# Optimization experiments

Hardware: AMD Instinct MI355X
Metric: run time of the kernel (lower is better)

## Reference

```python
import jax, jax.numpy as jnp
import numpy as np

BATCH, K, N, D = 8192, 8, 1024, 256
BETA = 0.25


def setup_inputs() -> dict:
    key = jax.random.key(0)
    kx, ke = jax.random.split(key)
    x = jax.random.normal(kx, (BATCH, K, D), dtype=jnp.float32)
    entries = jax.random.normal(ke, (K, N, D), dtype=jnp.float32)
    return {"x": x, "entries": entries}


def reference(x, entries):
    # x: [b, k, d]; entries: [k, n, d]
    xt = jnp.transpose(x, (1, 0, 2))  # [k, b, d]
    # squared euclidean distances (argmin is identical to cdist argmin)
    d2 = (
        jnp.sum(xt * xt, axis=-1)[:, :, None]
        + jnp.sum(entries * entries, axis=-1)[:, None, :]
        - 2.0 * jnp.einsum("kbd,knd->kbn", xt, entries)
    )  # [k, b, n]
    idx = jnp.argmin(d2, axis=-1)  # [k, b]
    quantized = jnp.take_along_axis(entries, idx[:, :, None], axis=1)  # [k, b, d]
    quantized = jnp.transpose(quantized, (1, 0, 2))  # [b, k, d]
    # straight-through estimator
    x_q = x + jax.lax.stop_gradient(quantized - x)
    dictionary_loss = jnp.mean(
        jnp.sum((jax.lax.stop_gradient(x) - quantized) ** 2, axis=-1)
    )
    commitment_loss = BETA * jnp.mean(
        jnp.sum((x - jax.lax.stop_gradient(quantized)) ** 2, axis=-1)
    )
    return x_q, jnp.transpose(idx, (1, 0)), dictionary_loss, commitment_loss
```

## Files before the change

kernel.cpp:

```cpp
#include <hip/hip_runtime.h>
#include <cstdint>
#include <cstddef>

#define BATCH 8192
#define KC 8
#define NC 1024
#define DC 256
#define TAU 0.10f

typedef __attribute__((ext_vector_type(8))) _Float16 half8;
typedef __attribute__((ext_vector_type(4))) _Float16 half4;
typedef __attribute__((ext_vector_type(4))) float floatx4;

__device__ __forceinline__ void async_load16(const void* g, void* l) {
    __builtin_amdgcn_global_load_lds((const __attribute__((address_space(1))) uint32_t*)g,
                                     (__attribute__((address_space(3))) uint32_t*)l, 16, 0, 0);
}

__device__ __forceinline__ int lidx(int r, int c) {
    return (r >> 3) * 1024 + (r & 7) * 128 + ((c ^ (r & 7)) * 16);
}
__device__ __forceinline__ half8 ldsr(const char* base, int r, int c) {
    return *(const half8*)(base + lidx(r, c));
}

__global__ __launch_bounds__(256) void prep_e_kernel(const float* __restrict__ entries,
                                                     _Float16* __restrict__ Ecat,
                                                     float* __restrict__ eef) {
    int wave = threadIdx.x >> 6, lane = threadIdx.x & 63;
    int row = blockIdx.x * 4 + wave;
    float4 v = ((const float4*)(entries + (size_t)row * DC))[lane];
    half4 h;
    h.x = (_Float16)v.x; h.y = (_Float16)v.y; h.z = (_Float16)v.z; h.w = (_Float16)v.w;
    *(half4*)(Ecat + (size_t)row * 256 + lane * 4) = h;
    double s = (double)v.x * v.x + (double)v.y * v.y + (double)v.z * v.z + (double)v.w * v.w;
    #pragma unroll
    for (int off = 32; off > 0; off >>= 1) s += __shfl_down(s, off, 64);
    if (lane == 0) eef[row] = (float)s;
}

__global__ __launch_bounds__(256, 2) void vq_gemm(const float* __restrict__ x,
                                                  const float* __restrict__ entries,
                                                  const _Float16* __restrict__ Ecat,
                                                  const float* __restrict__ eef,
                                                  float* __restrict__ out_idx,
                                                  float* __restrict__ out_q,
                                                  double* __restrict__ partial,
                                                  int* __restrict__ flag_list,
                                                  int* __restrict__ flag_cnt) {
    __shared__ alignas(16) char Bst[2][32768];
    __shared__ float eef_lds[NC];
    __shared__ float tv1[128];
    __shared__ float tv2[128];
    __shared__ int   ti1[128];
    __shared__ int   idx_lds[128];
    __shared__ double red[256];

    const int t = threadIdx.x;
    const int k  = blockIdx.x & 7;
    const int b0 = (blockIdx.x >> 3) * 128;
    const int w = t >> 6, lane = t & 63;
    const int quad = lane >> 4, col = lane & 15;
    const int rl = lane >> 3;
    const int cs = (lane & 7) ^ rl;

    { float4 v = ((const float4*)(eef + (size_t)k * NC))[t]; *(float4*)(eef_lds + t * 4) = v; }

    half8 Ah[2][8];
    #pragma unroll
    for (int mi = 0; mi < 2; ++mi) {
        const float* xrow = x + ((size_t)(b0 + w * 32 + mi * 16 + col) * KC + k) * DC + quad * 8;
        #pragma unroll
        for (int ks = 0; ks < 8; ++ks) {
            float4 u0 = *(const float4*)(xrow + ks * 32);
            float4 u1 = *(const float4*)(xrow + ks * 32 + 4);
            float f[8] = {u0.x, u0.y, u0.z, u0.w, u1.x, u1.y, u1.z, u1.w};
            half8 h;
            #pragma unroll
            for (int j = 0; j < 8; ++j) h[j] = (_Float16)f[j];
            Ah[mi][ks] = h;
        }
    }

    const char* EcatK = (const char*)(Ecat + (size_t)k * NC * 256);

    #define ISSUE_B(nt_, h_)                                                             \
        {                                                                                \
            char* bb_ = Bst[h_];                                                         \
            _Pragma("unroll")                                                            \
            for (int j = 0; j < 8; ++j) {                                                \
                int li_ = w * 8 + j; int sub_ = li_ >> 4, grp_ = li_ & 15;               \
                const char* src_ = EcatK + (size_t)((nt_) * 128 + grp_ * 8 + rl) * 512   \
                                 + ((h_) * 128 + sub_ * 64) * 2 + cs * 16;               \
                async_load16(src_, bb_ + sub_ * 16384 + grp_ * 1024 + lane * 16);        \
            }                                                                            \
        }

    #define STAGE(h_, DOISS_, nti_)                                                      \
        {                                                                                \
            asm volatile("s_waitcnt vmcnt(0)" ::: "memory");                             \
            __builtin_amdgcn_s_barrier();                                                \
            __builtin_amdgcn_sched_barrier(0);                                           \
            if (DOISS_) { ISSUE_B((nti_), (h_) ^ 1); }                                   \
            const char* Bs_ = Bst[h_];                                                   \
            __builtin_amdgcn_s_setprio(1);                                               \
            _Pragma("unroll")                                                            \
            for (int sub = 0; sub < 2; ++sub) {                                          \
                _Pragma("unroll")                                                        \
                for (int kk = 0; kk < 2; ++kk) {                                         \
                    const int cb = kk * 4 + quad;                                        \
                    _Pragma("unroll")                                                    \
                    for (int ni = 0; ni < 8; ++ni) {                                     \
                        half8 bh = ldsr(Bs_ + sub * 16384, ni * 16 + col, cb);           \
                        acc[0][ni] = __builtin_amdgcn_mfma_f32_16x16x32_f16(             \
                            Ah[0][(h_) * 4 + sub * 2 + kk], bh, acc[0][ni], 0, 0, 0);    \
                        acc[1][ni] = __builtin_amdgcn_mfma_f32_16x16x32_f16(             \
                            Ah[1][(h_) * 4 + sub * 2 + kk], bh, acc[1][ni], 0, 0, 0);    \
                    }                                                                    \
                }                                                                        \
            }                                                                            \
            __builtin_amdgcn_s_setprio(0);                                               \
        }

    float lv1[8], lv2[8]; int li1[8];
    #pragma unroll
    for (int q = 0; q < 8; ++q) { lv1[q] = 1e30f; lv2[q] = 1e30f; li1[q] = 0; }

    ISSUE_B(0, 0);

    for (int nt = 0; nt < 8; ++nt) {
        const int n0 = nt * 128;
        floatx4 acc[2][8] = {};
        STAGE(0, 1, nt)
        STAGE(1, (nt < 7), nt + 1)
        float ev[8];
        #pragma unroll
        for (int ni = 0; ni < 8; ++ni) ev[ni] = eef_lds[n0 + ni * 16 + col];
        #pragma unroll
        for (int mi = 0; mi < 2; ++mi) {
            #pragma unroll
            for (int reg = 0; reg < 4; ++reg) {
                const int q = mi * 4 + reg;
                #pragma unroll
                for (int ni = 0; ni < 8; ++ni) {
                    float val = fmaf(-2.0f, acc[mi][ni][reg], ev[ni]);
                    int n = n0 + ni * 16 + col;
                    bool lt1 = val < lv1[q];
                    bool lt2 = val < lv2[q];
                    float nv2 = lt1 ? lv1[q] : (lt2 ? val : lv2[q]);
                    li1[q] = lt1 ? n : li1[q];
                    lv1[q] = lt1 ? val : lv1[q];
                    lv2[q] = nv2;
                }
            }
        }
    }

    #pragma unroll
    for (int mi = 0; mi < 2; ++mi) {
        #pragma unroll
        for (int reg = 0; reg < 4; ++reg) {
            const int q = mi * 4 + reg;
            float v1 = lv1[q], v2 = lv2[q]; int i1 = li1[q];
            #pragma unroll
            for (int off = 1; off < 16; off <<= 1) {
                float o1 = __shfl_xor(v1, off, 16);
                float o2 = __shfl_xor(v2, off, 16);
                int   oi = __shfl_xor(i1, off, 16);
                bool sw = o1 < v1;
                float hi = sw ? v1 : o1;
                v1 = sw ? o1 : v1;
                i1 = sw ? oi : i1;
                v2 = fminf(fminf(v2, o2), hi);
            }
            if (col == 0) {
                int row = w * 32 + mi * 16 + quad * 4 + reg;
                tv1[row] = v1; tv2[row] = v2; ti1[row] = i1;
            }
        }
    }

    __syncthreads();
    if (t < 128) {
        float v1 = tv1[t], v2 = tv2[t];
        int rid = (b0 + t) * KC + k;
        if (v2 - v1 < TAU) {
            int pos = atomicAdd(&flag_cnt[k], 1);
            flag_list[k * 8192 + pos] = rid;
            idx_lds[t] = -1;
        } else {
            int n = ti1[t];
            idx_lds[t] = n;
            out_idx[rid] = (float)n;
        }
    }
    __syncthreads();

    double s = 0.0;
    #pragma unroll
    for (int rr = 0; rr < 8; ++rr) {
        int r = rr * 16 + (t >> 4);
        int c = t & 15;
        int n = idx_lds[r];
        if (n >= 0) {
            const float4* xp = (const float4*)(x + ((size_t)(b0 + r) * KC + k) * DC);
            const float4* ep = (const float4*)(entries + ((size_t)k * NC + n) * DC);
            float4* op = (float4*)(out_q + ((size_t)(b0 + r) * KC + k) * DC);
            #pragma unroll
            for (int j = 0; j < 4; ++j) {
                int ci = j * 16 + c;
                float4 xv = xp[ci], evv = ep[ci];
                op[ci] = evv;
                double d0 = (double)xv.x - evv.x, d1 = (double)xv.y - evv.y;
                double d2 = (double)xv.z - evv.z, d3 = (double)xv.w - evv.w;
                s += d0 * d0 + d1 * d1 + d2 * d2 + d3 * d3;
            }
        }
    }
    red[t] = s;
    __syncthreads();
    for (int off2 = 128; off2 > 0; off2 >>= 1) {
        if (t < off2) red[t] += red[t + off2];
        __syncthreads();
    }
    if (t == 0) partial[blockIdx.x] = red[0];
    #undef STAGE
    #undef ISSUE_B
}

__global__ __launch_bounds__(256) void refine_scan(const float* __restrict__ x,
                                                   const float* __restrict__ entries,
                                                   const int* __restrict__ flag_list,
                                                   const int* __restrict__ flag_cnt,
                                                   unsigned long long* __restrict__ slots) {
    __shared__ alignas(16) char tileb[128 * 256];
    __shared__ float xs[16 * 260];
    const int t = threadIdx.x;
    const int r = t >> 4, eg = t & 15;
    for (int it = blockIdx.x; it < 8 * 8 * 512; it += gridDim.x) {
        const int k = it & 7, seg = (it >> 3) & 7, g = it >> 6;
        const int cnt_k = flag_cnt[k];
        if (g * 16 >= cnt_k) continue;
        const int nrows = min(16, cnt_k - g * 16);
        const int myrow = (r < nrows) ? r : 0;
        const int rid = flag_list[k * 8192 + g * 16 + myrow];
        {
            const int rr = t >> 4, c16 = t & 15;
            const int rid2 = flag_list[k * 8192 + g * 16 + ((rr < nrows) ? rr : 0)];
            const float4* xp = (const float4*)(x + (size_t)rid2 * DC);
            #pragma unroll
            for (int j = 0; j < 4; ++j) {
                float4 v = xp[c16 * 4 + j];
                *(float4*)(xs + rr * 260 + (c16 * 4 + j) * 4) = v;
            }
        }
        double acc[8] = {};
        #pragma unroll
        for (int c = 0; c < 4; ++c) {
            {
                const int c16 = t & 15;
                #pragma unroll
                for (int it2 = 0; it2 < 8; ++it2) {
                    int row = it2 * 16 + (t >> 4);
                    float4 v = *(const float4*)(entries
                        + ((size_t)k * NC + seg * 128 + row) * DC + c * 64 + c16 * 4);
                    *(float4*)(tileb + row * 256 + ((c16 ^ (row >> 3)) * 16)) = v;
                }
            }
            __syncthreads();
            const float* xpp = xs + r * 260 + c * 64;
            #pragma unroll 4
            for (int dq = 0; dq < 16; ++dq) {
                float4 xv = *(const float4*)(xpp + dq * 4);
                #pragma unroll
                for (int j = 0; j < 8; ++j) {
                    int e = eg * 8 + j;
                    float4 evv = *(const float4*)(tileb + e * 256 + ((dq ^ eg) * 16));
                    double d0 = (double)xv.x - (double)evv.x;
                    double d1 = (double)xv.y - (double)evv.y;
                    double d2 = (double)xv.z - (double)evv.z;
                    double d3 = (double)xv.w - (double)evv.w;
                    acc[j] += d0 * d0 + d1 * d1 + d2 * d2 + d3 * d3;
                }
            }
            __syncthreads();
        }
        double best = acc[0]; int bn = seg * 128 + eg * 8;
        #pragma unroll
        for (int j = 1; j < 8; ++j) {
            if (acc[j] < best) { best = acc[j]; bn = seg * 128 + eg * 8 + j; }
        }
        unsigned long long key =
            ((unsigned long long)__double_as_longlong(best) & ~1023ull)
            | (unsigned long long)(unsigned)bn;
        #pragma unroll
        for (int off = 1; off < 16; off <<= 1) {
            unsigned long long o = __shfl_xor(key, off, 16);
            key = o < key ? o : key;
        }
        if (eg == 0 && r < nrows) {
            atomicMin(&slots[k * 8192 + g * 16 + r], key);
        }
        (void)rid;
    }
}

__global__ __launch_bounds__(256) void refine_pick(const float* __restrict__ entries,
                                                   const int* __restrict__ flag_list,
                                                   const int* __restrict__ flag_cnt,
                                                   const unsigned long long* __restrict__ slots,
                                                   float* __restrict__ out_idx,
                                                   float* __restrict__ out_q,
                                                   double* __restrict__ refAcc) {
    const int t = threadIdx.x;
    for (int idx = blockIdx.x; idx < 8 * 8192; idx += gridDim.x) {
        const int k = idx >> 13, pos = idx & 8191;
        if (pos >= flag_cnt[k]) continue;
        unsigned long long key = slots[idx];
        int n = (int)(key & 1023ull);
        int rid = flag_list[idx];
        out_q[(size_t)rid * DC + t] = entries[((size_t)k * NC + n) * DC + t];
        if (t == 0) {
            out_idx[rid] = (float)n;
            atomicAdd(refAcc, __longlong_as_double((long long)(key & ~1023ull)));
        }
    }
}

__global__ __launch_bounds__(256) void finalize_kernel(const double* __restrict__ partial,
                                                       const double* __restrict__ refAcc,
                                                       float* __restrict__ out) {
    __shared__ double red[256];
    const int t = threadIdx.x;
    double s = 0.0;
    for (int i = t; i < 512; i += 256) s += partial[i];
    red[t] = s;
    __syncthreads();
    for (int off = 128; off > 0; off >>= 1) {
        if (t < off) red[t] += red[t + off];
        __syncthreads();
    }
    if (t == 0) {
        double L = (red[0] + *refAcc) * (1.0 / 65536.0);
        out[(size_t)BATCH * KC * DC + BATCH * KC + 0] = (float)L;
        out[(size_t)BATCH * KC * DC + BATCH * KC + 1] = (float)(0.25 * L);
    }
}

extern "C" void kernel_launch(void* const* d_in, const int* in_sizes, int n_in,
                              void* d_out, int out_size, void* d_ws, size_t ws_size,
                              hipStream_t stream) {
    const float* x       = (const float*)d_in[0];
    const float* entries = (const float*)d_in[1];
    float* out = (float*)d_out;

    char* ws = (char*)d_ws;
    int*      flag_cnt  = (int*)ws;
    double*   refAcc    = (double*)(ws + 64);
    double*   partial   = (double*)(ws + 4096);
    float*    eef       = (float*)(ws + 65536);
    int*      flag_list = (int*)(ws + 131072);
    _Float16* Ecat      = (_Float16*)(ws + 1048576);
    unsigned long long* slots = (unsigned long long*)(ws + 5242880);

    float* out_q   = out;
    float* out_idx = out + (size_t)BATCH * KC * DC;

    hipMemsetAsync(ws, 0, 128, stream);
    hipMemsetAsync(slots, 0xFF, (size_t)65536 * 8, stream);
    prep_e_kernel<<<KC * NC / 4, 256, 0, stream>>>(entries, Ecat, eef);
    vq_gemm<<<512, 256, 0, stream>>>(x, entries, Ecat, eef, out_idx, out_q,
                                     partial, flag_list, flag_cnt);
    refine_scan<<<512, 256, 0, stream>>>(x, entries, flag_list, flag_cnt, slots);
    refine_pick<<<512, 256, 0, stream>>>(entries, flag_list, flag_cnt, slots,
                                         out_idx, out_q, refAcc);
    finalize_kernel<<<1, 256, 0, stream>>>(partial, refAcc, out);
}
```

Measured before the change: 225.9 us.

## Split codebook N across two blocks and resolve top-2 in a separate kernel

The GEMM kernel now covers half of the codebook per block, so the grid doubles to 1024 blocks. Shared memory per block is halved, allowing three blocks per CU instead of two. Each half writes its best candidate as a sortable key and atomically updates a global second-best minimum. A new resolve kernel merges the two halves, applies the ambiguity threshold, and writes the quantized output and loss partials. The aim is better occupancy and load balance, at the cost of an extra launch, an extra memset, and each block reloading the same x rows.

```diff
diff --git a/kernel.cpp b/kernel.cpp
--- a/kernel.cpp
+++ b/kernel.cpp
@@ -15,6 +15,14 @@
 __device__ __forceinline__ void async_load16(const void* g, void* l) {
     __builtin_amdgcn_global_load_lds((const __attribute__((address_space(1))) uint32_t*)g,
                                      (__attribute__((address_space(3))) uint32_t*)l, 16, 0, 0);
+}
+__device__ __forceinline__ unsigned sortable(float v) {
+    unsigned u = __float_as_uint(v);
+    return u ^ (unsigned)(((int)u >> 31) | 0x80000000);
+}
+__device__ __forceinline__ float unsortable(unsigned ks) {
+    unsigned u = (ks & 0x80000000u) ? (ks ^ 0x80000000u) : ~ks;
+    return __uint_as_float(u);
 }
 
 __device__ __forceinline__ int lidx(int r, int c) {
@@ -39,32 +47,26 @@
     if (lane == 0) eef[row] = (float)s;
 }
 
-__global__ __launch_bounds__(256, 2) void vq_gemm(const float* __restrict__ x,
-                                                  const float* __restrict__ entries,
+__global__ __launch_bounds__(256, 3) void vq_gemm(const float* __restrict__ x,
                                                   const _Float16* __restrict__ Ecat,
                                                   const float* __restrict__ eef,
-                                                  float* __restrict__ out_idx,
-                                                  float* __restrict__ out_q,
-                                                  double* __restrict__ partial,
-                                                  int* __restrict__ flag_list,
-                                                  int* __restrict__ flag_cnt) {
-    __shared__ alignas(16) char Bst[2][32768];
-    __shared__ float eef_lds[NC];
-    __shared__ float tv1[128];
-    __shared__ float tv2[128];
-    __shared__ int   ti1[128];
-    __shared__ int   idx_lds[128];
-    __shared__ double red[256];
+                                                  unsigned long long* __restrict__ s01,
+                                                  unsigned* __restrict__ g2min) {
+    __shared__ alignas(16) char Bst[2][16384];
+    __shared__ float eef_lds[512];
 
     const int t = threadIdx.x;
     const int k  = blockIdx.x & 7;
-    const int b0 = (blockIdx.x >> 3) * 128;
+    const int g  = blockIdx.x >> 3;
+    const int b0 = (g >> 1) * 128;
+    const int nh = g & 1;
+    const int ncol0 = nh * 512;
     const int w = t >> 6, lane = t & 63;
     const int quad = lane >> 4, col = lane & 15;
     const int rl = lane >> 3;
     const int cs = (lane & 7) ^ rl;
 
-    { float4 v = ((const float4*)(eef + (size_t)k * NC))[t]; *(float4*)(eef_lds + t * 4) = v; }
+    ((float2*)eef_lds)[t] = ((const float2*)(eef + (size_t)k * NC + ncol0))[t];
 
     half8 Ah[2][8];
     #pragma unroll
@@ -84,39 +86,37 @@
 
     const char* EcatK = (const char*)(Ecat + (size_t)k * NC * 256);
 
-    #define ISSUE_B(nt_, h_)                                                             \
+    #define ISSUE_B(nt_, ds_, buf_)                                                      \
         {                                                                                \
-            char* bb_ = Bst[h_];                                                         \
+            char* bb_ = Bst[buf_];                                                       \
             _Pragma("unroll")                                                            \
-            for (int j = 0; j < 8; ++j) {                                                \
-                int li_ = w * 8 + j; int sub_ = li_ >> 4, grp_ = li_ & 15;               \
-                const char* src_ = EcatK + (size_t)((nt_) * 128 + grp_ * 8 + rl) * 512   \
-                                 + ((h_) * 128 + sub_ * 64) * 2 + cs * 16;               \
-                async_load16(src_, bb_ + sub_ * 16384 + grp_ * 1024 + lane * 16);        \
+            for (int j = 0; j < 4; ++j) {                                                \
+                int grp_ = w * 4 + j;                                                    \
+                const char* src_ = EcatK                                                 \
+                    + (size_t)(ncol0 + (nt_) * 128 + grp_ * 8 + rl) * 512                \
+                    + (ds_) * 128 + cs * 16;                                             \
+                async_load16(src_, bb_ + grp_ * 1024 + lane * 16);                       \
             }                                                                            \
         }
 
-    #define STAGE(h_, DOISS_, nti_)                                                      \
+    #define STAGE(nt_, ds_, DOISS_, nnt_, nds_)                                          \
         {                                                                                \
             asm volatile("s_waitcnt vmcnt(0)" ::: "memory");                             \
             __builtin_amdgcn_s_barrier();                                                \
             __builtin_amdgcn_sched_barrier(0);                                           \
-            if (DOISS_) { ISSUE_B((nti_), (h_) ^ 1); }                                   \
-            const char* Bs_ = Bst[h_];                                                   \
+            if (DOISS_) { ISSUE_B((nnt_), (nds_), ((ds_) + 1) & 1); }                    \
+            const char* Bs_ = Bst[(ds_) & 1];                                            \
             __builtin_amdgcn_s_setprio(1);                                               \
             _Pragma("unroll")                                                            \
-            for (int sub = 0; sub < 2; ++sub) {                                          \
+            for (int kk = 0; kk < 2; ++kk) {                                             \
+                const int cb = kk * 4 + quad;                                            \
                 _Pragma("unroll")                                                        \
-                for (int kk = 0; kk < 2; ++kk) {                                         \
-                    const int cb = kk * 4 + quad;                                        \
-                    _Pragma("unroll")                                                    \
-                    for (int ni = 0; ni < 8; ++ni) {                                     \
-                        half8 bh = ldsr(Bs_ + sub * 16384, ni * 16 + col, cb);           \
-                        acc[0][ni] = __builtin_amdgcn_mfma_f32_16x16x32_f16(             \
-                            Ah[0][(h_) * 4 + sub * 2 + kk], bh, acc[0][ni], 0, 0, 0);    \
-                        acc[1][ni] = __builtin_amdgcn_mfma_f32_16x16x32_f16(             \
-                            Ah[1][(h_) * 4 + sub * 2 + kk], bh, acc[1][ni], 0, 0, 0);    \
-                    }                                                                    \
+                for (int ni = 0; ni < 8; ++ni) {                                         \
+                    half8 bh = ldsr(Bs_, ni * 16 + col, cb);                             \
+                    acc[0][ni] = __builtin_amdgcn_mfma_f32_16x16x32_f16(                 \
+                        Ah[0][(ds_) * 2 + kk], bh, acc[0][ni], 0, 0, 0);                 \
+                    acc[1][ni] = __builtin_amdgcn_mfma_f32_16x16x32_f16(                 \
+                        Ah[1][(ds_) * 2 + kk], bh, acc[1][ni], 0, 0, 0);                 \
                 }                                                                        \
             }                                                                            \
             __builtin_amdgcn_s_setprio(0);                                               \
@@ -126,13 +126,15 @@
     #pragma unroll
     for (int q = 0; q < 8; ++q) { lv1[q] = 1e30f; lv2[q] = 1e30f; li1[q] = 0; }
 
-    ISSUE_B(0, 0);
-
-    for (int nt = 0; nt < 8; ++nt) {
+    ISSUE_B(0, 0, 0);
+
+    for (int nt = 0; nt < 4; ++nt) {
         const int n0 = nt * 128;
         floatx4 acc[2][8] = {};
-        STAGE(0, 1, nt)
-        STAGE(1, (nt < 7), nt + 1)
+        STAGE(nt, 0, 1, nt, 1)
+        STAGE(nt, 1, 1, nt, 2)
+        STAGE(nt, 2, 1, nt, 3)
+        STAGE(nt, 3, (nt < 3), nt + 1, 0)
         float ev[8];
         #pragma unroll
         for (int ni = 0; ni < 8; ++ni) ev[ni] = eef_lds[n0 + ni * 16 + col];
@@ -157,39 +159,63 @@
     }
 
     #pragma unroll
-    for (int mi = 0; mi < 2; ++mi) {
-        #pragma unroll
-        for (int reg = 0; reg < 4; ++reg) {
-            const int q = mi * 4 + reg;
-            float v1 = lv1[q], v2 = lv2[q]; int i1 = li1[q];
-            #pragma unroll
-            for (int off = 1; off < 16; off <<= 1) {
-                float o1 = __shfl_xor(v1, off, 16);
-                float o2 = __shfl_xor(v2, off, 16);
-                int   oi = __shfl_xor(i1, off, 16);
-                bool sw = o1 < v1;
-                float hi = sw ? v1 : o1;
-                v1 = sw ? o1 : v1;
-                i1 = sw ? oi : i1;
-                v2 = fminf(fminf(v2, o2), hi);
-            }
-            if (col == 0) {
-                int row = w * 32 + mi * 16 + quad * 4 + reg;
-                tv1[row] = v1; tv2[row] = v2; ti1[row] = i1;
-            }
-        }
-    }
-
-    __syncthreads();
+    for (int q = 0; q < 8; ++q) {
+        float v1 = lv1[q], v2 = lv2[q]; int i1 = li1[q];
+        #pragma unroll
+        for (int off = 1; off < 16; off <<= 1) {
+            float o1 = __shfl_xor(v1, off, 16);
+            float o2 = __shfl_xor(v2, off, 16);
+            int   oi = __shfl_xor(i1, off, 16);
+            bool sw = o1 < v1;
+            float hi = sw ? v1 : o1;
+            v1 = sw ? o1 : v1;
+            i1 = sw ? oi : i1;
+            v2 = fminf(fminf(v2, o2), hi);
+        }
+        if (col == 0) {
+            const int mi = q >> 2, reg = q & 3;
+            int row = w * 32 + mi * 16 + quad * 4 + reg;
+            int rid = (b0 + row) * KC + k;
+            s01[(size_t)nh * 65536 + rid] =
+                ((unsigned long long)sortable(v1) << 32) | (unsigned)(ncol0 + i1);
+            atomicMin(&g2min[rid], sortable(v2));
+        }
+    }
+    #undef STAGE
+    #undef ISSUE_B
+}
+
+__global__ __launch_bounds__(256) void resolve_kernel(const float* __restrict__ x,
+                                                      const float* __restrict__ entries,
+                                                      const unsigned long long* __restrict__ s01,
+                                                      const unsigned* __restrict__ g2min,
+                                                      float* __restrict__ out_idx,
+                                                      float* __restrict__ out_q,
+                                                      double* __restrict__ partial,
+                                                      int* __restrict__ flag_list,
+                                                      int* __restrict__ flag_cnt) {
+    __shared__ int idx_lds[128];
+    __shared__ double red[256];
+    const int t = threadIdx.x;
+    const int r0 = blockIdx.x * 128;
+
     if (t < 128) {
-        float v1 = tv1[t], v2 = tv2[t];
-        int rid = (b0 + t) * KC + k;
+        int rid = r0 + t;
+        unsigned long long sa = s01[rid], sb = s01[65536 + rid];
+        unsigned long long lo = sa < sb ? sa : sb;
+        unsigned long long hi = sa < sb ? sb : sa;
+        unsigned v2u = g2min[rid];
+        unsigned hv = (unsigned)(hi >> 32);
+        if (hv < v2u) v2u = hv;
+        float v1 = unsortable((unsigned)(lo >> 32));
+        float v2 = unsortable(v2u);
         if (v2 - v1 < TAU) {
+            int k = rid & 7;
             int pos = atomicAdd(&flag_cnt[k], 1);
             flag_list[k * 8192 + pos] = rid;
             idx_lds[t] = -1;
         } else {
-            int n = ti1[t];
+            int n = (int)(lo & 0xFFFFFFFFull);
             idx_lds[t] = n;
             out_idx[rid] = (float)n;
         }
@@ -203,9 +229,10 @@
         int c = t & 15;
         int n = idx_lds[r];
         if (n >= 0) {
-            const float4* xp = (const float4*)(x + ((size_t)(b0 + r) * KC + k) * DC);
-            const float4* ep = (const float4*)(entries + ((size_t)k * NC + n) * DC);
-            float4* op = (float4*)(out_q + ((size_t)(b0 + r) * KC + k) * DC);
+            int rid2 = r0 + r;
+            const float4* xp = (const float4*)(x + (size_t)rid2 * DC);
+            const float4* ep = (const float4*)(entries + (((size_t)(rid2 & 7)) * NC + n) * DC);
+            float4* op = (float4*)(out_q + (size_t)rid2 * DC);
             #pragma unroll
             for (int j = 0; j < 4; ++j) {
                 int ci = j * 16 + c;
@@ -224,8 +251,6 @@
         __syncthreads();
     }
     if (t == 0) partial[blockIdx.x] = red[0];
-    #undef STAGE
-    #undef ISSUE_B
 }
 
 __global__ __launch_bounds__(256) void refine_scan(const float* __restrict__ x,
@@ -242,8 +267,6 @@
         const int cnt_k = flag_cnt[k];
         if (g * 16 >= cnt_k) continue;
         const int nrows = min(16, cnt_k - g * 16);
-        const int myrow = (r < nrows) ? r : 0;
-        const int rid = flag_list[k * 8192 + g * 16 + myrow];
         {
             const int rr = t >> 4, c16 = t & 15;
             const int rid2 = flag_list[k * 8192 + g * 16 + ((rr < nrows) ? rr : 0)];
@@ -301,7 +324,6 @@
         if (eg == 0 && r < nrows) {
             atomicMin(&slots[k * 8192 + g * 16 + r], key);
         }
-        (void)rid;
     }
 }
 
@@ -362,15 +384,19 @@
     int*      flag_list = (int*)(ws + 131072);
     _Float16* Ecat      = (_Float16*)(ws + 1048576);
     unsigned long long* slots = (unsigned long long*)(ws + 5242880);
+    unsigned* g2min     = (unsigned*)(ws + 5767168);
+    unsigned long long* s01 = (unsigned long long*)(ws + 6291456);
 
     float* out_q   = out;
     float* out_idx = out + (size_t)BATCH * KC * DC;
 
     hipMemsetAsync(ws, 0, 128, stream);
     hipMemsetAsync(slots, 0xFF, (size_t)65536 * 8, stream);
+    hipMemsetAsync(g2min, 0xFF, (size_t)65536 * 4, stream);
     prep_e_kernel<<<KC * NC / 4, 256, 0, stream>>>(entries, Ecat, eef);
-    vq_gemm<<<512, 256, 0, stream>>>(x, entries, Ecat, eef, out_idx, out_q,
-                                     partial, flag_list, flag_cnt);
+    vq_gemm<<<1024, 256, 0, stream>>>(x, Ecat, eef, s01, g2min);
+    resolve_kernel<<<512, 256, 0, stream>>>(x, entries, s01, g2min, out_idx,
+                                            out_q, partial, flag_list, flag_cnt);
     refine_scan<<<512, 256, 0, stream>>>(x, entries, flag_list, flag_cnt, slots);
     refine_pick<<<512, 256, 0, stream>>>(entries, flag_list, flag_cnt, slots,
                                          out_idx, out_q, refAcc);
```

Result: slower. 299.5 us (+32.6%).
